# Kernel tuning notes

Hardware: AMD Instinct MI355X
Metric: run time of the kernel (lower is better)

The kernel has to match this reference:

```python
import jax, jax.numpy as jnp
import numpy as np

GRID = (128, 128)
LR = 0.1
SIGMA = 3.0


def setup_inputs() -> dict:
    key = jax.random.key(0)
    k1, k2 = jax.random.split(key)
    x = jax.random.normal(k1, (4096, 256), dtype=jnp.float32)
    weights = jax.random.normal(k2, (128, 128, 256), dtype=jnp.float32)
    return {"x": x, "weights": weights}


def reference(x, weights):
    """One SOM training step: find BMU for each sample, then apply the
    Gaussian-neighborhood weight update (mean over the batch).
    Returns the updated weights [R, C, D]."""
    B, D = x.shape
    R, C, _ = weights.shape

    # ---- forward / find_bmu: squared distances x -> all neurons ----
    w_flat = weights.reshape(R * C, D)                     # [N, D]
    d2 = (jnp.sum(x * x, axis=1)[:, None]
          + jnp.sum(w_flat * w_flat, axis=1)[None, :]
          - 2.0 * x @ w_flat.T)                            # [B, N]
    bmu_idx = jnp.argmin(d2, axis=1)                       # [B]
    bmu_rows = bmu_idx // C                                # [B]
    bmu_cols = bmu_idx % C                                 # [B]

    # ---- update_weights: Gaussian neighborhood around each BMU ----
    rows = jnp.arange(R, dtype=jnp.float32)                # grid coords
    cols = jnp.arange(C, dtype=jnp.float32)
    dr2 = (rows[None, :] - bmu_rows[:, None].astype(jnp.float32)) ** 2  # [B, R]
    dc2 = (cols[None, :] - bmu_cols[:, None].astype(jnp.float32)) ** 2  # [B, C]
    neuron_dists = dr2[:, :, None] + dc2[:, None, :]       # [B, R, C]
    neigh = jnp.exp(-neuron_dists / (2.0 * SIGMA ** 2))    # [B, R, C]

    # mean_b lr*neigh[b,r,c]*(x[b,d] - w[r,c,d])  without a [B,R,C,D] tensor
    num = jnp.einsum('brc,bd->rcd', neigh, x)              # [R, C, D]
    neigh_sum = jnp.sum(neigh, axis=0)                     # [R, C]
    delta_mean = (LR / B) * (num - neigh_sum[:, :, None] * weights)
    return weights + delta_mean
```

## Files before the change

kernel.cpp:

```cpp
#include <hip/hip_runtime.h>

typedef _Float16 f16;
typedef _Float16 f16x8 __attribute__((ext_vector_type(8)));
typedef _Float16 f16x4 __attribute__((ext_vector_type(4)));
typedef float f32x4 __attribute__((ext_vector_type(4)));

#define GLL(gp, lp) __builtin_amdgcn_global_load_lds( \
    (const __attribute__((address_space(1))) void*)(gp), \
    (__attribute__((address_space(3))) void*)(lp), 16, 0, 0)

__global__ void prep_w_kernel(const float* __restrict__ w, f16* __restrict__ whi,
                              f16* __restrict__ wlo, float* __restrict__ wnorm) {
    int wv = blockIdx.x * 4 + (threadIdx.x >> 6);
    int lane = threadIdx.x & 63;
    float4 v = reinterpret_cast<const float4*>(w + (size_t)wv * 256)[lane];
    float vv[4] = {v.x, v.y, v.z, v.w};
    f16x4 h, l;
    float ss = 0.f;
#pragma unroll
    for (int i = 0; i < 4; i++) {
        f16 hh = (f16)vv[i];
        h[i] = hh;
        l[i] = (f16)(vv[i] - (float)hh);
        ss += vv[i] * vv[i];
    }
    *(f16x4*)(whi + (size_t)wv * 256 + lane * 4) = h;
    *(f16x4*)(wlo + (size_t)wv * 256 + lane * 4) = l;
#pragma unroll
    for (int off = 32; off > 0; off >>= 1) ss += __shfl_down(ss, off);
    if (lane == 0) wnorm[wv] = ss;
}

__global__ void prep_x_kernel(const float* __restrict__ x, f16* __restrict__ xhi,
                              f16* __restrict__ xlo, unsigned long long* __restrict__ bmu) {
    const int t = blockIdx.x * 256 + threadIdx.x;
    if (blockIdx.x < 16) bmu[blockIdx.x * 256 + threadIdx.x] = ~0ull;
    float4 v = reinterpret_cast<const float4*>(x)[t];
    float vv[4] = {v.x, v.y, v.z, v.w};
    f16x4 h, l;
#pragma unroll
    for (int i = 0; i < 4; i++) {
        f16 hh = (f16)vv[i];
        h[i] = hh;
        l[i] = (f16)(vv[i] - (float)hh);
    }
    *(f16x4*)(xhi + (size_t)t * 4) = h;
    *(f16x4*)(xlo + (size_t)t * 4) = l;
}

__launch_bounds__(256, 4)
__global__ void gemm_argmin_kernel(const f16* __restrict__ xhi, const f16* __restrict__ xlo,
                                   const f16* __restrict__ whi, const f16* __restrict__ wlo,
                                   const float* __restrict__ wnorm,
                                   unsigned long long* __restrict__ bmu) {
    __shared__ f16 As[128][64];
    __shared__ f16 Bs[128][64];
    __shared__ float s_wn[128];
    const int m0 = blockIdx.x * 128;
    const int n0 = blockIdx.y * 128;
    const int tid = threadIdx.x;
    const int lane = tid & 63, wid = tid >> 6;
    const int wm = wid >> 1, wn = wid & 1;
    const int l15 = lane & 15, l4 = lane >> 4;
    const int swz = (l15 & 7) << 3;
    if (tid < 128) s_wn[tid] = wnorm[n0 + tid];
    f32x4 acc[4][4] = {};
    for (int kt = 0; kt < 768; kt += 64) {
        const f16* asrc = (kt >= 512) ? xlo : xhi;
        const f16* bsrc = (kt >= 256 && kt < 512) ? wlo : whi;
        const int kk = kt & 255;
        __syncthreads();
#pragma unroll
        for (int q = 0; q < 4; q++) {
            int off = tid * 16 + q * 4096;
            int row = off >> 7;
            int colh = ((off & 127) ^ ((row & 7) << 4)) >> 1;
            GLL(asrc + (size_t)(m0 + row) * 256 + kk + colh, (char*)(&As[0][0]) + off);
        }
#pragma unroll
        for (int q = 0; q < 4; q++) {
            int off = tid * 16 + q * 4096;
            int row = off >> 7;
            int colh = ((off & 127) ^ ((row & 7) << 4)) >> 1;
            GLL(bsrc + (size_t)(n0 + row) * 256 + kk + colh, (char*)(&Bs[0][0]) + off);
        }
        __syncthreads();
#pragma unroll
        for (int ks = 0; ks < 2; ks++) {
            f16x8 af[4], bf[4];
#pragma unroll
            for (int i = 0; i < 4; i++)
                af[i] = *(const f16x8*)&As[wm * 64 + i * 16 + l15][(ks * 32 + l4 * 8) ^ swz];
#pragma unroll
            for (int i = 0; i < 4; i++)
                bf[i] = *(const f16x8*)&Bs[wn * 64 + i * 16 + l15][(ks * 32 + l4 * 8) ^ swz];
#pragma unroll
            for (int i = 0; i < 4; i++)
#pragma unroll
                for (int j = 0; j < 4; j++)
                    acc[i][j] = __builtin_amdgcn_mfma_f32_16x16x32_f16(af[i], bf[j], acc[i][j], 0, 0, 0);
        }
    }
#pragma unroll
    for (int mi = 0; mi < 4; mi++) {
#pragma unroll
        for (int j = 0; j < 4; j++) {
            float best = 1e30f;
            int bidx = 0x7fffffff;
#pragma unroll
            for (int ni = 0; ni < 4; ni++) {
                int nl = wn * 64 + ni * 16 + l15;
                float v = s_wn[nl] - 2.0f * acc[mi][ni][j];
                int g = n0 + nl;
                if (v < best || (v == best && g < bidx)) { best = v; bidx = g; }
            }
#pragma unroll
            for (int off = 1; off < 16; off <<= 1) {
                float ov = __shfl_xor(best, off);
                int oi = __shfl_xor(bidx, off);
                if (ov < best || (ov == best && oi < bidx)) { best = ov; bidx = oi; }
            }
            if (l15 == 0) {
                unsigned u = __float_as_uint(best);
                u = (u & 0x80000000u) ? ~u : (u | 0x80000000u);
                unsigned long long key = ((unsigned long long)u << 32) | (unsigned)bidx;
                int m = m0 + wm * 64 + mi * 16 + l4 * 4 + j;
                atomicMin(&bmu[m], key);
            }
        }
    }
}

__global__ void zeroS_kernel(float4* __restrict__ S4, float4* __restrict__ count4) {
    const int t = blockIdx.x * 256 + threadIdx.x;
    S4[t] = float4{0.f, 0.f, 0.f, 0.f};
    if (blockIdx.x < 16) count4[t] = float4{0.f, 0.f, 0.f, 0.f};
}

__global__ void scatter_kernel(const float* __restrict__ x,
                               const unsigned long long* __restrict__ bmu,
                               float* __restrict__ S, float* __restrict__ count) {
    const int b = blockIdx.x * 4 + (threadIdx.x >> 6);
    const int lane = threadIdx.x & 63;
    const int n = (int)(bmu[b] & 0xffffffffull);
    float4 v = reinterpret_cast<const float4*>(x + (size_t)b * 256)[lane];
    float* dst = S + (size_t)n * 256 + lane * 4;
    atomicAdd(dst + 0, v.x);
    atomicAdd(dst + 1, v.y);
    atomicAdd(dst + 2, v.z);
    atomicAdd(dst + 3, v.w);
    if (lane == 0) atomicAdd(count + n, 1.0f);
}

__global__ void ns_pass1_kernel(const float* __restrict__ count, float* __restrict__ cnt_r) {
    __shared__ float g[128];
    const int r = blockIdx.x;
    const int bc = threadIdx.x;
    g[bc] = expf(-(float)(bc * bc) / 18.0f);
    __syncthreads();
    float acc = 0.f;
    for (int br = 0; br < 128; br++) {
        int dd = br - r; dd = dd < 0 ? -dd : dd;
        acc += g[dd] * count[br * 128 + bc];
    }
    cnt_r[r * 128 + bc] = acc;
}

__global__ void conv_r_kernel(const float* __restrict__ S, float* __restrict__ T1, int h) {
    __shared__ float tile[128][64];
    __shared__ float g[128];
    const int tid = threadIdx.x;
    const int j0 = blockIdx.x * 64;
    if (tid < 128) g[tid] = expf(-(float)(tid * tid) / 18.0f);
    const int jbase = (j0 >> 7) * 256 + h * 128 + (j0 & 127);
#pragma unroll
    for (int q = 0; q < 8; q++) {
        int off = tid * 16 + q * 4096;
        int row = off >> 8;
        int col = (off & 255) >> 2;
        GLL(S + (size_t)row * 32768 + jbase + col, (char*)(&tile[0][0]) + off);
    }
    __syncthreads();
    const int jg = (tid & 15) * 4;
    const int r0 = (tid >> 4) * 8;
    f32x4 acc[8] = {};
    for (int br = 0; br < 128; br++) {
        f32x4 v = *(const f32x4*)&tile[br][jg];
#pragma unroll
        for (int i = 0; i < 8; i++) {
            int dd = br - (r0 + i); dd = dd < 0 ? -dd : dd;
            acc[i] += g[dd] * v;
        }
    }
#pragma unroll
    for (int i = 0; i < 8; i++)
        *(f32x4*)&T1[(size_t)(r0 + i) * 16384 + j0 + jg] = acc[i];
}

__global__ void conv_c_kernel(const float* __restrict__ T1, const float* __restrict__ cnt_r,
                              const float* __restrict__ w, float* __restrict__ out, int h) {
    __shared__ float tile[128][64];
    __shared__ float g[128];
    __shared__ float s_cnt[128];
    __shared__ float s_ns[128];
    const int tid = threadIdx.x;
    const int r = blockIdx.x;
    const int d0 = blockIdx.y * 64;
    if (tid < 128) g[tid] = expf(-(float)(tid * tid) / 18.0f);
    if (tid >= 128 && tid < 256) s_cnt[tid - 128] = cnt_r[r * 128 + (tid - 128)];
#pragma unroll
    for (int q = 0; q < 8; q++) {
        int off = tid * 16 + q * 4096;
        int row = off >> 8;
        int col = (off & 255) >> 2;
        GLL(T1 + (size_t)r * 16384 + (size_t)row * 128 + d0 + col, (char*)(&tile[0][0]) + off);
    }
    __syncthreads();
    if (tid < 128) {
        float acc = 0.f;
        for (int bc = 0; bc < 128; bc++) {
            int dd = tid - bc; dd = dd < 0 ? -dd : dd;
            acc += g[dd] * s_cnt[bc];
        }
        s_ns[tid] = acc;
    }
    __syncthreads();
    const int jg = (tid & 15) * 4;
    const int c0 = (tid >> 4) * 8;
    f32x4 acc[8] = {};
    for (int bc = 0; bc < 128; bc++) {
        f32x4 v = *(const f32x4*)&tile[bc][jg];
#pragma unroll
        for (int i = 0; i < 8; i++) {
            int dd = bc - (c0 + i); dd = dd < 0 ? -dd : dd;
            acc[i] += g[dd] * v;
        }
    }
    const float s = 0.1f / 4096.0f;
#pragma unroll
    for (int i = 0; i < 8; i++) {
        size_t gi = ((size_t)(r * 128 + c0 + i)) * 256 + h * 128 + d0 + jg;
        f32x4 wv = *(const f32x4*)&w[gi];
        f32x4 o = wv + s * (acc[i] - s_ns[c0 + i] * wv);
        *(f32x4*)&out[gi] = o;
    }
}

extern "C" void kernel_launch(void* const* d_in, const int* in_sizes, int n_in,
                              void* d_out, int out_size, void* d_ws, size_t ws_size,
                              hipStream_t stream) {
    const float* x = (const float*)d_in[0];
    const float* w = (const float*)d_in[1];
    float* out = (float*)d_out;
    char* ws = (char*)d_ws;

    f16* whi = (f16*)(ws + 0);
    f16* wlo = (f16*)(ws + 8388608);
    float* S = (float*)(ws + 0);
    f16* xhi = (f16*)(ws + 16777216);
    f16* xlo = (f16*)(ws + 18874368);
    float* wnorm = (float*)(ws + 20971520);
    float* T1 = (float*)(ws + 16777216);
    unsigned long long* bmu = (unsigned long long*)(ws + 25165824);
    float* count = (float*)(ws + 25198592);
    float* cnt_r = (float*)(ws + 25264128);

    prep_w_kernel<<<4096, 256, 0, stream>>>(w, whi, wlo, wnorm);
    prep_x_kernel<<<1024, 256, 0, stream>>>(x, xhi, xlo, bmu);
    gemm_argmin_kernel<<<dim3(32, 128), 256, 0, stream>>>(xhi, xlo, whi, wlo, wnorm, bmu);
    zeroS_kernel<<<4096, 256, 0, stream>>>((float4*)S, (float4*)count);
    scatter_kernel<<<1024, 256, 0, stream>>>(x, bmu, S, count);
    ns_pass1_kernel<<<128, 128, 0, stream>>>(count, cnt_r);
    conv_r_kernel<<<256, 256, 0, stream>>>(S, T1, 0);
    conv_c_kernel<<<dim3(128, 2), 256, 0, stream>>>(T1, cnt_r, w, out, 0);
    conv_r_kernel<<<256, 256, 0, stream>>>(S, T1, 1);
    conv_c_kernel<<<dim3(128, 2), 256, 0, stream>>>(T1, cnt_r, w, out, 1);
}
```

Before: 306.2 us.

## Store separable-conv intermediate in fp16 and merge prep and conv launches

Fuses the weight and input prep kernels into one launch that also zeroes the count buffer. The row-convolution intermediate T1 is stored as fp16, which halves its memory traffic. That lets the whole feature dimension fit in one pass, so the two half-width conv_r/conv_c launch pairs become one pair. This reduces launch count and intermediate bandwidth, at the cost of fp16 rounding in the neighbourhood-weighted sums.

```diff
diff --git a/kernel.cpp b/kernel.cpp
--- a/kernel.cpp
+++ b/kernel.cpp
@@ -9,43 +9,49 @@
     (const __attribute__((address_space(1))) void*)(gp), \
     (__attribute__((address_space(3))) void*)(lp), 16, 0, 0)
 
-__global__ void prep_w_kernel(const float* __restrict__ w, f16* __restrict__ whi,
-                              f16* __restrict__ wlo, float* __restrict__ wnorm) {
-    int wv = blockIdx.x * 4 + (threadIdx.x >> 6);
-    int lane = threadIdx.x & 63;
-    float4 v = reinterpret_cast<const float4*>(w + (size_t)wv * 256)[lane];
-    float vv[4] = {v.x, v.y, v.z, v.w};
-    f16x4 h, l;
-    float ss = 0.f;
-#pragma unroll
-    for (int i = 0; i < 4; i++) {
-        f16 hh = (f16)vv[i];
-        h[i] = hh;
-        l[i] = (f16)(vv[i] - (float)hh);
-        ss += vv[i] * vv[i];
-    }
-    *(f16x4*)(whi + (size_t)wv * 256 + lane * 4) = h;
-    *(f16x4*)(wlo + (size_t)wv * 256 + lane * 4) = l;
-#pragma unroll
-    for (int off = 32; off > 0; off >>= 1) ss += __shfl_down(ss, off);
-    if (lane == 0) wnorm[wv] = ss;
-}
-
-__global__ void prep_x_kernel(const float* __restrict__ x, f16* __restrict__ xhi,
-                              f16* __restrict__ xlo, unsigned long long* __restrict__ bmu) {
-    const int t = blockIdx.x * 256 + threadIdx.x;
-    if (blockIdx.x < 16) bmu[blockIdx.x * 256 + threadIdx.x] = ~0ull;
-    float4 v = reinterpret_cast<const float4*>(x)[t];
-    float vv[4] = {v.x, v.y, v.z, v.w};
-    f16x4 h, l;
-#pragma unroll
-    for (int i = 0; i < 4; i++) {
-        f16 hh = (f16)vv[i];
-        h[i] = hh;
-        l[i] = (f16)(vv[i] - (float)hh);
-    }
-    *(f16x4*)(xhi + (size_t)t * 4) = h;
-    *(f16x4*)(xlo + (size_t)t * 4) = l;
+__global__ void prep_kernel(const float* __restrict__ w, const float* __restrict__ x,
+                            f16* __restrict__ whi, f16* __restrict__ wlo,
+                            float* __restrict__ wnorm, f16* __restrict__ xhi,
+                            f16* __restrict__ xlo, unsigned long long* __restrict__ bmu,
+                            float4* __restrict__ count4) {
+    const int bid = blockIdx.x;
+    const int tid = threadIdx.x;
+    if (bid < 4096) {
+        int wv = bid * 4 + (tid >> 6);
+        int lane = tid & 63;
+        float4 v = reinterpret_cast<const float4*>(w + (size_t)wv * 256)[lane];
+        float vv[4] = {v.x, v.y, v.z, v.w};
+        f16x4 h, l;
+        float ss = 0.f;
+#pragma unroll
+        for (int i = 0; i < 4; i++) {
+            f16 hh = (f16)vv[i];
+            h[i] = hh;
+            l[i] = (f16)(vv[i] - (float)hh);
+            ss += vv[i] * vv[i];
+        }
+        *(f16x4*)(whi + (size_t)wv * 256 + lane * 4) = h;
+        *(f16x4*)(wlo + (size_t)wv * 256 + lane * 4) = l;
+#pragma unroll
+        for (int off = 32; off > 0; off >>= 1) ss += __shfl_down(ss, off);
+        if (lane == 0) wnorm[wv] = ss;
+    } else {
+        const int xb = bid - 4096;
+        if (xb < 16) bmu[xb * 256 + tid] = ~0ull;
+        else if (xb < 32) count4[(xb - 16) * 256 + tid] = float4{0.f, 0.f, 0.f, 0.f};
+        const int t = xb * 256 + tid;
+        float4 v = reinterpret_cast<const float4*>(x)[t];
+        float vv[4] = {v.x, v.y, v.z, v.w};
+        f16x4 h, l;
+#pragma unroll
+        for (int i = 0; i < 4; i++) {
+            f16 hh = (f16)vv[i];
+            h[i] = hh;
+            l[i] = (f16)(vv[i] - (float)hh);
+        }
+        *(f16x4*)(xhi + (size_t)t * 4) = h;
+        *(f16x4*)(xlo + (size_t)t * 4) = l;
+    }
 }
 
 __launch_bounds__(256, 4)
@@ -131,10 +137,9 @@
     }
 }
 
-__global__ void zeroS_kernel(float4* __restrict__ S4, float4* __restrict__ count4) {
+__global__ void zeroS_kernel(float4* __restrict__ S4) {
     const int t = blockIdx.x * 256 + threadIdx.x;
     S4[t] = float4{0.f, 0.f, 0.f, 0.f};
-    if (blockIdx.x < 16) count4[t] = float4{0.f, 0.f, 0.f, 0.f};
 }
 
 __global__ void scatter_kernel(const float* __restrict__ x,
@@ -166,19 +171,18 @@
     cnt_r[r * 128 + bc] = acc;
 }
 
-__global__ void conv_r_kernel(const float* __restrict__ S, float* __restrict__ T1, int h) {
+__global__ void conv_r_kernel(const float* __restrict__ S, f16* __restrict__ T1) {
     __shared__ float tile[128][64];
     __shared__ float g[128];
     const int tid = threadIdx.x;
     const int j0 = blockIdx.x * 64;
     if (tid < 128) g[tid] = expf(-(float)(tid * tid) / 18.0f);
-    const int jbase = (j0 >> 7) * 256 + h * 128 + (j0 & 127);
 #pragma unroll
     for (int q = 0; q < 8; q++) {
         int off = tid * 16 + q * 4096;
         int row = off >> 8;
         int col = (off & 255) >> 2;
-        GLL(S + (size_t)row * 32768 + jbase + col, (char*)(&tile[0][0]) + off);
+        GLL(S + (size_t)row * 32768 + j0 + col, (char*)(&tile[0][0]) + off);
     }
     __syncthreads();
     const int jg = (tid & 15) * 4;
@@ -193,13 +197,17 @@
         }
     }
 #pragma unroll
-    for (int i = 0; i < 8; i++)
-        *(f32x4*)&T1[(size_t)(r0 + i) * 16384 + j0 + jg] = acc[i];
-}
-
-__global__ void conv_c_kernel(const float* __restrict__ T1, const float* __restrict__ cnt_r,
-                              const float* __restrict__ w, float* __restrict__ out, int h) {
-    __shared__ float tile[128][64];
+    for (int i = 0; i < 8; i++) {
+        f16x4 hv;
+#pragma unroll
+        for (int k = 0; k < 4; k++) hv[k] = (f16)acc[i][k];
+        *(f16x4*)&T1[(size_t)(r0 + i) * 32768 + j0 + jg] = hv;
+    }
+}
+
+__global__ void conv_c_kernel(const f16* __restrict__ T1, const float* __restrict__ cnt_r,
+                              const float* __restrict__ w, float* __restrict__ out) {
+    __shared__ f16 tile[128][64];
     __shared__ float g[128];
     __shared__ float s_cnt[128];
     __shared__ float s_ns[128];
@@ -209,11 +217,11 @@
     if (tid < 128) g[tid] = expf(-(float)(tid * tid) / 18.0f);
     if (tid >= 128 && tid < 256) s_cnt[tid - 128] = cnt_r[r * 128 + (tid - 128)];
 #pragma unroll
-    for (int q = 0; q < 8; q++) {
+    for (int q = 0; q < 4; q++) {
         int off = tid * 16 + q * 4096;
-        int row = off >> 8;
-        int col = (off & 255) >> 2;
-        GLL(T1 + (size_t)r * 16384 + (size_t)row * 128 + d0 + col, (char*)(&tile[0][0]) + off);
+        int row = off >> 7;
+        int colh = (off & 127) >> 1;
+        GLL(T1 + (size_t)r * 32768 + (size_t)row * 256 + d0 + colh, (char*)(&tile[0][0]) + off);
     }
     __syncthreads();
     if (tid < 128) {
@@ -229,7 +237,8 @@
     const int c0 = (tid >> 4) * 8;
     f32x4 acc[8] = {};
     for (int bc = 0; bc < 128; bc++) {
-        f32x4 v = *(const f32x4*)&tile[bc][jg];
+        f16x4 hv = *(const f16x4*)&tile[bc][jg];
+        f32x4 v = {(float)hv[0], (float)hv[1], (float)hv[2], (float)hv[3]};
 #pragma unroll
         for (int i = 0; i < 8; i++) {
             int dd = bc - (c0 + i); dd = dd < 0 ? -dd : dd;
@@ -239,7 +248,7 @@
     const float s = 0.1f / 4096.0f;
 #pragma unroll
     for (int i = 0; i < 8; i++) {
-        size_t gi = ((size_t)(r * 128 + c0 + i)) * 256 + h * 128 + d0 + jg;
+        size_t gi = ((size_t)(r * 128 + c0 + i)) * 256 + d0 + jg;
         f32x4 wv = *(const f32x4*)&w[gi];
         f32x4 o = wv + s * (acc[i] - s_ns[c0 + i] * wv);
         *(f32x4*)&out[gi] = o;
@@ -260,19 +269,17 @@
     f16* xhi = (f16*)(ws + 16777216);
     f16* xlo = (f16*)(ws + 18874368);
     float* wnorm = (float*)(ws + 20971520);
-    float* T1 = (float*)(ws + 16777216);
+    f16* T1 = (f16*)(ws + 16777216);
     unsigned long long* bmu = (unsigned long long*)(ws + 25165824);
     float* count = (float*)(ws + 25198592);
     float* cnt_r = (float*)(ws + 25264128);
 
-    prep_w_kernel<<<4096, 256, 0, stream>>>(w, whi, wlo, wnorm);
-    prep_x_kernel<<<1024, 256, 0, stream>>>(x, xhi, xlo, bmu);
+    prep_kernel<<<5120, 256, 0, stream>>>(w, x, whi, wlo, wnorm, xhi, xlo, bmu,
+                                          (float4*)count);
     gemm_argmin_kernel<<<dim3(32, 128), 256, 0, stream>>>(xhi, xlo, whi, wlo, wnorm, bmu);
-    zeroS_kernel<<<4096, 256, 0, stream>>>((float4*)S, (float4*)count);
+    zeroS_kernel<<<4096, 256, 0, stream>>>((float4*)S);
     scatter_kernel<<<1024, 256, 0, stream>>>(x, bmu, S, count);
     ns_pass1_kernel<<<128, 128, 0, stream>>>(count, cnt_r);
-    conv_r_kernel<<<256, 256, 0, stream>>>(S, T1, 0);
-    conv_c_kernel<<<dim3(128, 2), 256, 0, stream>>>(T1, cnt_r, w, out, 0);
-    conv_r_kernel<<<256, 256, 0, stream>>>(S, T1, 1);
-    conv_c_kernel<<<dim3(128, 2), 256, 0, stream>>>(T1, cnt_r, w, out, 1);
-}
+    conv_r_kernel<<<512, 256, 0, stream>>>(S, T1);
+    conv_c_kernel<<<dim3(128, 4), 256, 0, stream>>>(T1, cnt_r, w, out);
+}
```

Measured after the change: 283.2 us. 7.5% less time.
